# Kernel tuning notes

Hardware: AMD Instinct MI355X
Metric: run time of the kernel (lower is better)

The kernel has to match this reference:

```python
import jax, jax.numpy as jnp
import numpy as np

N_LEVELS = 16
N_FEATS = 2
LOG2_T = 19
BASE_RES = 16.0
FINEST_RES = 512.0
N_POINTS = 1_000_000
HASH_MASK = np.uint32((1 << LOG2_T) - 1)
PRIME1 = np.uint32(2654435761)  # second spatial-hash prime (first is 1)


def setup_inputs() -> dict:
    key = jax.random.key(0)
    k1, k2 = jax.random.split(key)
    x = jax.random.uniform(k1, (N_POINTS, 2), dtype=jnp.float32)
    # nn.init.uniform_(w, -1e-4, 1e-4) per level, stacked: [L, T, F]
    embeddings = (jax.random.uniform(k2, (N_LEVELS, 2 ** LOG2_T, N_FEATS), dtype=jnp.float32) * 2.0 - 1.0) * 1e-4
    return {"x": x, "embeddings": embeddings}


def reference(x, embeddings):
    L = N_LEVELS
    n = x.shape[0]
    # per-level resolutions: floor(base * b**i)
    b = np.exp((np.log(FINEST_RES) - np.log(BASE_RES)) / (L - 1))
    res = np.floor(BASE_RES * b ** np.arange(L)).astype(np.float32)  # [L]
    res_j = jnp.asarray(res)

    pixels = x[None, :, :] * res_j[:, None, None]           # [L, n, 2]
    top_left = jnp.floor(pixels).astype(jnp.int32)          # [L, n, 2]
    offsets = jnp.array([[0, 0], [1, 0], [0, 1], [1, 1]], dtype=jnp.int32)
    box = top_left[:, :, None, :] + offsets[None, None]     # [L, n, 4, 2]
    box = jnp.clip(box, 0, res_j[:, None, None, None].astype(jnp.int32))

    # spatial hash: (c0*1 ^ c1*prime) & mask, with uint32 wraparound like torch int32
    c = box.astype(jnp.uint32)
    addr = ((c[..., 0] * np.uint32(1)) ^ (c[..., 1] * PRIME1)) & HASH_MASK  # [L, n, 4]
    addr = addr.astype(jnp.int32)

    # gather per-level corner features: [L, n, 4, F]
    feats = jax.vmap(lambda table, idx: table[idx])(embeddings, addr)

    # bilinear interpolation
    w = pixels - jnp.floor(pixels)                          # [L, n, 2]
    w0 = w[..., 0:1]
    w1 = w[..., 1:2]
    f0, f1, f2, f3 = feats[:, :, 0], feats[:, :, 1], feats[:, :, 2], feats[:, :, 3]
    f = (f0 * (1 - w0) + f1 * w0) * (1 - w1) + (f2 * (1 - w0) + f3 * w0) * w1  # [L, n, F]

    # concat levels along feature dim -> [n, L*F]
    return jnp.transpose(f, (1, 0, 2)).reshape(n, L * N_FEATS)
```

## Files before the change

### kernel.cpp

```cpp
#include <hip/hip_runtime.h>
#include <hip/hip_fp16.h>
#include <cmath>

#define NLVL 16
#define TSIZE (1u << 19)
#define HMASK ((1u << 19) - 1u)
#define PRIME1 2654435761u
#define FSCALE 1024.0f
#define FINV   (1.0f/1024.0f)

typedef float f32x4 __attribute__((ext_vector_type(4)));
typedef unsigned int       u32;
typedef unsigned long long u64;

struct Params {
    float rf[NLVL];
    int   ri[NLVL];
    int   base[NLVL];
    int   stride[NLVL];
};

__device__ __forceinline__ float2 h2f(u32 u) {
    __half2 h; __builtin_memcpy(&h, &u, 4);
    return __half22float2(h);
}

__global__ __launch_bounds__(256) void build_dense_q(
    const float2* __restrict__ emb, uint2* __restrict__ dense, Params p)
{
    const int l  = blockIdx.y;
    const int r  = blockIdx.x;
    const int ri = p.ri[l];
    if (r > ri) return;
    const unsigned hy0 = (unsigned)r * PRIME1;
    const unsigned hy1 = (unsigned)min(r + 1, ri) * PRIME1;
    const u64* tab = (const u64*)(emb + (size_t)l * TSIZE);
    uint2* drow = dense + p.base[l] + (size_t)r * p.stride[l];
    for (int cx = threadIdx.x; cx <= ri; cx += 256) {
        u64 raw0 = __builtin_nontemporal_load(tab + (((unsigned)cx ^ hy0) & HMASK));
        u64 raw1 = __builtin_nontemporal_load(tab + (((unsigned)cx ^ hy1) & HMASK));
        float2 v0, v1;
        __builtin_memcpy(&v0, &raw0, 8);
        __builtin_memcpy(&v1, &raw1, 8);
        uint2 e;
        e.x = (u32)__half_as_ushort(__float2half_rn(v0.x * FSCALE))
            | ((u32)__half_as_ushort(__float2half_rn(v0.y * FSCALE)) << 16);
        e.y = (u32)__half_as_ushort(__float2half_rn(v1.x * FSCALE))
            | ((u32)__half_as_ushort(__float2half_rn(v1.y * FSCALE)) << 16);
        drow[cx] = e;
    }
}

__global__ __launch_bounds__(256) void hash_embed_q(
    const float2* __restrict__ x,
    const uint2*  __restrict__ dense,
    float*        __restrict__ out,
    Params p, int n)
{
    __shared__ float lds[8 * 512];
    const int tid = threadIdx.x;
    const int i = blockIdx.x * 256 + tid;
    float2 xy = make_float2(0.f, 0.f);
    if (i < n) {
        u64 raw = __builtin_nontemporal_load((const u64*)(x + i));
        __builtin_memcpy(&xy, &raw, 8);
    }

    uint4 q[NLVL];
    float w0v[NLVL], w1v[NLVL];
    u32 edgemask = 0;

    #pragma unroll
    for (int l = 0; l < NLVL; ++l) {
        const float rf = p.rf[l];
        const int ri = p.ri[l];
        const float px = xy.x * rf, py = xy.y * rf;
        const float fx = floorf(px), fy = floorf(py);
        w0v[l] = px - fx;
        w1v[l] = py - fy;
        const int tx = (int)fx, ty = (int)fy;
        const int cx0 = min(tx, ri);
        const int cy0 = min(ty, ri);
        edgemask |= (u32)(cx0 == ri) << l;
        const uint2* a = dense + p.base[l] + cy0 * p.stride[l] + cx0;
        __builtin_memcpy(&q[l], a, 16);
    }
    __builtin_amdgcn_sched_barrier(0);

    const long long total = (long long)n * 32;
    const long long base  = (long long)blockIdx.x * 8192;

    #pragma unroll
    for (int half = 0; half < 2; ++half) {
        if (half == 1) __syncthreads();
        #pragma unroll
        for (int j = 0; j < 8; ++j) {
            const int l = half * 8 + j;
            const float w0 = w0v[l], w1 = w1v[l];
            const float u0 = 1.f - w0, u1 = 1.f - w1;
            const bool ed = (edgemask >> l) & 1u;
            const float2 e00 = h2f(q[l].x);
            const float2 e10 = h2f(q[l].y);
            const float2 e01 = h2f(ed ? q[l].x : q[l].z);
            const float2 e11 = h2f(ed ? q[l].y : q[l].w);
            const float g0 = ((e00.x*u0 + e01.x*w0)*u1 + (e10.x*u0 + e11.x*w0)*w1) * FINV;
            const float g1 = ((e00.y*u0 + e01.y*w0)*u1 + (e10.y*u0 + e11.y*w0)*w1) * FINV;
            const int idx = j * 512 + ((2 * tid) ^ (j << 1));
            lds[idx]     = g0;
            lds[idx + 1] = g1;
        }
        __syncthreads();

        #pragma unroll
        for (int it = 0; it < 4; ++it) {
            const int f  = (it * 256 + tid) * 4;
            const int p2 = f >> 4;
            const int kk = f & 15;
            const int lh = kk >> 1;
            const long long g = base + (long long)p2 * 32 + half * 16 + kk;
            if (g < total) {
                const int s0 = lh * 512       + ((2 * p2) ^ (lh << 1));
                const int s1 = (lh + 1) * 512 + ((2 * p2) ^ ((lh + 1) << 1));
                f32x4 v;
                v.x = lds[s0]; v.y = lds[s0 + 1];
                v.z = lds[s1]; v.w = lds[s1 + 1];
                __builtin_nontemporal_store(v, (f32x4*)(out + g));
            }
        }
    }
}

__global__ __launch_bounds__(256) void hash_embed_direct(
    const float2* __restrict__ x,
    const float2* __restrict__ emb,
    float* __restrict__ out,
    Params p, int n)
{
    __shared__ float2 lds[NLVL * 256];
    const int tid = threadIdx.x;
    const int i = blockIdx.x * 256 + tid;
    float2 xy = make_float2(0.f, 0.f);
    if (i < n) xy = x[i];

    #pragma unroll
    for (int half = 0; half < 2; ++half) {
        float2 f[32];
        float w0v[8], w1v[8];
        #pragma unroll
        for (int j = 0; j < 8; ++j) {
            const int l = half * 8 + j;
            const float rf = p.rf[l];
            const int ri = p.ri[l];
            const float px = xy.x * rf, py = xy.y * rf;
            const float fx = floorf(px), fy = floorf(py);
            w0v[j] = px - fx;
            w1v[j] = py - fy;
            const int tx = (int)fx, ty = (int)fy;
            const unsigned cx0 = (unsigned)min(tx, ri);
            const unsigned cy0 = (unsigned)min(ty, ri);
            const unsigned cx1 = (unsigned)min(tx + 1, ri);
            const unsigned cy1 = (unsigned)min(ty + 1, ri);
            const unsigned hy0 = cy0 * PRIME1;
            const unsigned hy1 = cy1 * PRIME1;
            const float2* tab = emb + (size_t)l * TSIZE;
            f[j*4+0] = tab[(cx0 ^ hy0) & HMASK];
            f[j*4+1] = tab[(cx1 ^ hy0) & HMASK];
            f[j*4+2] = tab[(cx0 ^ hy1) & HMASK];
            f[j*4+3] = tab[(cx1 ^ hy1) & HMASK];
        }
        #pragma unroll
        for (int j = 0; j < 8; ++j) {
            const int l = half * 8 + j;
            const float w0 = w0v[j], w1 = w1v[j];
            const float u0 = 1.f - w0, u1 = 1.f - w1;
            const float2 f0 = f[j*4+0], f1 = f[j*4+1], f2 = f[j*4+2], f3 = f[j*4+3];
            const float g0 = (f0.x*u0 + f1.x*w0)*u1 + (f2.x*u0 + f3.x*w0)*w1;
            const float g1 = (f0.y*u0 + f1.y*w0)*u1 + (f2.y*u0 + f3.y*w0)*w1;
            lds[l * 256 + tid] = make_float2(g0, g1);
        }
    }
    __syncthreads();

    const float* lf = (const float*)lds;
    const long long total = (long long)n * 32;
    const long long base = (long long)blockIdx.x * 8192;
    #pragma unroll
    for (int it = 0; it < 8; ++it) {
        const int k = (it * 256 + tid) * 4;
        if (base + k < total) {
            const int p2 = k >> 5;
            const int l0 = (k & 31) >> 1;
            float4 v;
            v.x = lf[(l0 * 256 + p2) * 2 + 0];
            v.y = lf[(l0 * 256 + p2) * 2 + 1];
            v.z = lf[((l0 + 1) * 256 + p2) * 2 + 0];
            v.w = lf[((l0 + 1) * 256 + p2) * 2 + 1];
            *(float4*)(out + base + k) = v;
        }
    }
}

extern "C" void kernel_launch(void* const* d_in, const int* in_sizes, int n_in,
                              void* d_out, int out_size, void* d_ws, size_t ws_size,
                              hipStream_t stream) {
    const float2* x = (const float2*)d_in[0];
    const float2* emb = (const float2*)d_in[1];
    float* out = (float*)d_out;
    const int n = in_sizes[0] / 2;

    Params p;
    int off = 0;
    const double b = std::exp((std::log(512.0) - std::log(16.0)) / 15.0);
    for (int l = 0; l < NLVL; ++l) {
        const double r = std::floor(16.0 * std::pow(b, (double)l));
        p.rf[l] = (float)r;
        p.ri[l] = (int)r;
        p.stride[l] = p.ri[l] + 2;
        p.base[l] = off;
        off += (p.ri[l] + 1) * (p.ri[l] + 2);
    }
    const size_t need = (size_t)off * sizeof(uint2);

    const int grid = (n + 255) / 256;
    if (ws_size >= need) {
        build_dense_q<<<dim3(513, 16), 256, 0, stream>>>(emb, (uint2*)d_ws, p);
        hash_embed_q<<<grid, 256, 0, stream>>>(x, (const uint2*)d_ws, out, p, n);
    } else {
        hash_embed_direct<<<grid, 256, 0, stream>>>(x, emb, out, p, n);
    }
}
```

Baseline: 231.2 us.

## Use compact single-row dense tables for the finest three levels

The finest three levels now store one packed half2 per grid cell in the dense table instead of a duplicated two-row quad, which halves that part of the table and the build kernel's writes. The main kernel loads two 8-byte rows for those levels instead of one 16-byte quad. Coarser levels keep the quad layout. The aim is to cut workspace size and cache footprint for the largest levels, at the price of one extra memory load per point per fine level.

```diff
diff --git a/kernel.cpp b/kernel.cpp
--- a/kernel.cpp
+++ b/kernel.cpp
@@ -3,6 +3,7 @@
 #include <cmath>
 
 #define NLVL 16
+#define QUAD_LVLS 13
 #define TSIZE (1u << 19)
 #define HMASK ((1u << 19) - 1u)
 #define PRIME1 2654435761u
@@ -25,35 +26,46 @@
     return __half22float2(h);
 }
 
-__global__ __launch_bounds__(256) void build_dense_q(
-    const float2* __restrict__ emb, uint2* __restrict__ dense, Params p)
+__device__ __forceinline__ u32 packh(float2 v) {
+    return (u32)__half_as_ushort(__float2half_rn(v.x * FSCALE))
+         | ((u32)__half_as_ushort(__float2half_rn(v.y * FSCALE)) << 16);
+}
+
+__global__ __launch_bounds__(256) void build_dense_hyb(
+    const float2* __restrict__ emb, u32* __restrict__ dense, Params p)
 {
     const int l  = blockIdx.y;
     const int r  = blockIdx.x;
     const int ri = p.ri[l];
     if (r > ri) return;
-    const unsigned hy0 = (unsigned)r * PRIME1;
-    const unsigned hy1 = (unsigned)min(r + 1, ri) * PRIME1;
     const u64* tab = (const u64*)(emb + (size_t)l * TSIZE);
-    uint2* drow = dense + p.base[l] + (size_t)r * p.stride[l];
-    for (int cx = threadIdx.x; cx <= ri; cx += 256) {
-        u64 raw0 = __builtin_nontemporal_load(tab + (((unsigned)cx ^ hy0) & HMASK));
-        u64 raw1 = __builtin_nontemporal_load(tab + (((unsigned)cx ^ hy1) & HMASK));
-        float2 v0, v1;
-        __builtin_memcpy(&v0, &raw0, 8);
-        __builtin_memcpy(&v1, &raw1, 8);
-        uint2 e;
-        e.x = (u32)__half_as_ushort(__float2half_rn(v0.x * FSCALE))
-            | ((u32)__half_as_ushort(__float2half_rn(v0.y * FSCALE)) << 16);
-        e.y = (u32)__half_as_ushort(__float2half_rn(v1.x * FSCALE))
-            | ((u32)__half_as_ushort(__float2half_rn(v1.y * FSCALE)) << 16);
-        drow[cx] = e;
-    }
-}
-
-__global__ __launch_bounds__(256) void hash_embed_q(
+    if (l < QUAD_LVLS) {
+        const unsigned hy0 = (unsigned)r * PRIME1;
+        const unsigned hy1 = (unsigned)min(r + 1, ri) * PRIME1;
+        uint2* drow = (uint2*)(dense + p.base[l]) + (size_t)r * p.stride[l];
+        for (int cx = threadIdx.x; cx <= ri; cx += 256) {
+            u64 raw0 = __builtin_nontemporal_load(tab + (((unsigned)cx ^ hy0) & HMASK));
+            u64 raw1 = __builtin_nontemporal_load(tab + (((unsigned)cx ^ hy1) & HMASK));
+            float2 v0, v1;
+            __builtin_memcpy(&v0, &raw0, 8);
+            __builtin_memcpy(&v1, &raw1, 8);
+            uint2 e; e.x = packh(v0); e.y = packh(v1);
+            drow[cx] = e;
+        }
+    } else {
+        const unsigned hy = (unsigned)r * PRIME1;
+        u32* drow = dense + p.base[l] + (size_t)r * p.stride[l];
+        for (int cx = threadIdx.x; cx <= ri; cx += 256) {
+            u64 raw = __builtin_nontemporal_load(tab + (((unsigned)cx ^ hy) & HMASK));
+            float2 v; __builtin_memcpy(&v, &raw, 8);
+            drow[cx] = packh(v);
+        }
+    }
+}
+
+__global__ __launch_bounds__(256) void hash_embed_hyb(
     const float2* __restrict__ x,
-    const uint2*  __restrict__ dense,
+    const u32*    __restrict__ dense,
     float*        __restrict__ out,
     Params p, int n)
 {
@@ -66,12 +78,13 @@
         __builtin_memcpy(&xy, &raw, 8);
     }
 
-    uint4 q[NLVL];
+    uint4 q[QUAD_LVLS];
+    uint2 pa[NLVL - QUAD_LVLS], pb[NLVL - QUAD_LVLS];
     float w0v[NLVL], w1v[NLVL];
     u32 edgemask = 0;
 
     #pragma unroll
-    for (int l = 0; l < NLVL; ++l) {
+    for (int l = 0; l < QUAD_LVLS; ++l) {
         const float rf = p.rf[l];
         const int ri = p.ri[l];
         const float px = xy.x * rf, py = xy.y * rf;
@@ -82,8 +95,26 @@
         const int cx0 = min(tx, ri);
         const int cy0 = min(ty, ri);
         edgemask |= (u32)(cx0 == ri) << l;
-        const uint2* a = dense + p.base[l] + cy0 * p.stride[l] + cx0;
+        const uint2* a = (const uint2*)(dense + p.base[l]) + cy0 * p.stride[l] + cx0;
         __builtin_memcpy(&q[l], a, 16);
+    }
+    #pragma unroll
+    for (int m = 0; m < NLVL - QUAD_LVLS; ++m) {
+        const int l = QUAD_LVLS + m;
+        const float rf = p.rf[l];
+        const int ri = p.ri[l];
+        const float px = xy.x * rf, py = xy.y * rf;
+        const float fx = floorf(px), fy = floorf(py);
+        w0v[l] = px - fx;
+        w1v[l] = py - fy;
+        const int tx = (int)fx, ty = (int)fy;
+        const int cx0 = min(tx, ri);
+        const int cy0 = min(ty, ri);
+        const int cy1 = min(ty + 1, ri);
+        edgemask |= (u32)(cx0 == ri) << l;
+        const u32* tab = dense + p.base[l];
+        __builtin_memcpy(&pa[m], tab + cy0 * p.stride[l] + cx0, 8);
+        __builtin_memcpy(&pb[m], tab + cy1 * p.stride[l] + cx0, 8);
     }
     __builtin_amdgcn_sched_barrier(0);
 
@@ -99,10 +130,19 @@
             const float w0 = w0v[l], w1 = w1v[l];
             const float u0 = 1.f - w0, u1 = 1.f - w1;
             const bool ed = (edgemask >> l) & 1u;
-            const float2 e00 = h2f(q[l].x);
-            const float2 e10 = h2f(q[l].y);
-            const float2 e01 = h2f(ed ? q[l].x : q[l].z);
-            const float2 e11 = h2f(ed ? q[l].y : q[l].w);
+            float2 e00, e01, e10, e11;
+            if (l < QUAD_LVLS) {
+                e00 = h2f(q[l].x);
+                e10 = h2f(q[l].y);
+                e01 = h2f(ed ? q[l].x : q[l].z);
+                e11 = h2f(ed ? q[l].y : q[l].w);
+            } else {
+                const int m = l - QUAD_LVLS;
+                e00 = h2f(pa[m].x);
+                e01 = h2f(ed ? pa[m].x : pa[m].y);
+                e10 = h2f(pb[m].x);
+                e11 = h2f(ed ? pb[m].x : pb[m].y);
+            }
             const float g0 = ((e00.x*u0 + e01.x*w0)*u1 + (e10.x*u0 + e11.x*w0)*w1) * FINV;
             const float g1 = ((e00.y*u0 + e01.y*w0)*u1 + (e10.y*u0 + e11.y*w0)*w1) * FINV;
             const int idx = j * 512 + ((2 * tid) ^ (j << 1));
@@ -217,14 +257,15 @@
         p.ri[l] = (int)r;
         p.stride[l] = p.ri[l] + 2;
         p.base[l] = off;
-        off += (p.ri[l] + 1) * (p.ri[l] + 2);
-    }
-    const size_t need = (size_t)off * sizeof(uint2);
+        const int cells = (p.ri[l] + 1) * (p.ri[l] + 2);
+        off += (l < QUAD_LVLS) ? cells * 2 : cells;
+    }
+    const size_t need = (size_t)off * sizeof(u32);
 
     const int grid = (n + 255) / 256;
     if (ws_size >= need) {
-        build_dense_q<<<dim3(513, 16), 256, 0, stream>>>(emb, (uint2*)d_ws, p);
-        hash_embed_q<<<grid, 256, 0, stream>>>(x, (const uint2*)d_ws, out, p, n);
+        build_dense_hyb<<<dim3(513, 16), 256, 0, stream>>>(emb, (u32*)d_ws, p);
+        hash_embed_hyb<<<grid, 256, 0, stream>>>(x, (const u32*)d_ws, out, p, n);
     } else {
         hash_embed_direct<<<grid, 256, 0, stream>>>(x, emb, out, p, n);
     }
```

Result: no change. 234.7 us (+1.5%).
